# Kernel tuning notes

Hardware: AMD Instinct MI355X
Metric: run time of the kernel (lower is better)

## Reference

```python
import jax, jax.numpy as jnp
import numpy as np

NUM_K_HEADS = 16
NUM_V_HEADS = 32
DK = 128
DV = 128
KCONV = 4
EPS = 1e-6
KEY_DIM = NUM_K_HEADS * DK      # 2048
VALUE_DIM = NUM_V_HEADS * DV    # 4096
HIDDEN = 2048
T_TOKENS = 4096


def setup_inputs() -> dict:
    key = jax.random.key(0)
    ks = jax.random.split(key, 10)
    s = 0.02
    return {
        "hidden_states": jax.random.normal(ks[0], (T_TOKENS, HIDDEN), jnp.float32),
        "W_qkv": jax.random.normal(ks[1], (2 * KEY_DIM + VALUE_DIM, HIDDEN), jnp.float32) * s,
        "W_z": jax.random.normal(ks[2], (VALUE_DIM, HIDDEN), jnp.float32) * s,
        "W_b": jax.random.normal(ks[3], (NUM_V_HEADS, HIDDEN), jnp.float32) * s,
        "W_a": jax.random.normal(ks[4], (NUM_V_HEADS, HIDDEN), jnp.float32) * s,
        "conv_weight": jax.random.normal(ks[5], (2 * KEY_DIM + VALUE_DIM, KCONV), jnp.float32) * 0.2,
        "dt_bias": jnp.ones((NUM_V_HEADS,), jnp.float32),
        "A_log": jax.random.normal(ks[6], (NUM_V_HEADS,), jnp.float32) * 0.5,
        "norm_weight": jnp.ones((DV,), jnp.float32),
        "W_out": jax.random.normal(ks[7], (HIDDEN, VALUE_DIM), jnp.float32) * s,
    }


def _l2norm(x):
    return x * jax.lax.rsqrt(jnp.sum(x * x, axis=-1, keepdims=True) + 1e-6)


def _gdn_forward(hidden_states, W_qkv, W_z, W_b, W_a, conv_weight,
                 dt_bias, A_log, norm_weight, W_out):
    T = hidden_states.shape[0]
    # input projections
    mixed_qkv = hidden_states @ W_qkv.T                         # [T, 2K+V]
    z = (hidden_states @ W_z.T).reshape(T, NUM_V_HEADS, DV)     # gate
    b = hidden_states @ W_b.T                                   # [T, Hv]
    a = hidden_states @ W_a.T                                   # [T, Hv]

    # depthwise causal conv1d (kernel 4) + silu, no bias
    xp = jnp.pad(mixed_qkv, ((KCONV - 1, 0), (0, 0)))
    conv = sum(xp[i:i + T] * conv_weight[:, i] for i in range(KCONV))
    x = jax.nn.silu(conv)

    q = x[:, :KEY_DIM].reshape(T, NUM_K_HEADS, DK)
    k = x[:, KEY_DIM:2 * KEY_DIM].reshape(T, NUM_K_HEADS, DK)
    v = x[:, 2 * KEY_DIM:].reshape(T, NUM_V_HEADS, DV)

    rep = NUM_V_HEADS // NUM_K_HEADS  # grouped value attention: repeat q/k heads
    q = jnp.repeat(_l2norm(q), rep, axis=1)  # [T, Hv, DK]
    k = jnp.repeat(_l2norm(k), rep, axis=1)

    beta = jax.nn.sigmoid(b)                                   # [T, Hv]
    g = -jnp.exp(A_log) * jax.nn.softplus(a + dt_bias)         # [T, Hv] log-decay
    scale = DK ** -0.5

    def step(S, inp):
        qt, kt, vt, bt, gt = inp
        S = S * jnp.exp(gt)[:, None, None]                     # gated decay
        kv = jnp.einsum('hk,hkv->hv', kt, S)                   # memory readout
        delta = (vt - kv) * bt[:, None]                        # delta rule update
        S = S + jnp.einsum('hk,hv->hkv', kt, delta)
        ot = jnp.einsum('hk,hkv->hv', qt, S) * scale
        return S, ot

    S0 = jnp.zeros((NUM_V_HEADS, DK, DV), mixed_qkv.dtype)
    _, o = jax.lax.scan(step, S0, (q, k, v, beta, g))          # o: [T, Hv, DV]

    # gated RMSNorm (norm before gate)
    var = jnp.mean(o * o, axis=-1, keepdims=True)
    on = o * jax.lax.rsqrt(var + EPS) * norm_weight
    y = on * jax.nn.silu(z)

    return y.reshape(T, VALUE_DIM) @ W_out.T                   # [T, HIDDEN]


def reference(hidden_states, W_qkv, W_z, W_b, W_a, conv_weight,
              dt_bias, A_log, norm_weight, W_out):
    return _gdn_forward(hidden_states, W_qkv, W_z, W_b, W_a, conv_weight,
                        dt_bias, A_log, norm_weight, W_out)
```

## Files before the change

kernel.cpp:

```cpp
#include <hip/hip_runtime.h>
#include <cstdint>
#include <cstddef>

typedef __bf16 bf16_t;
typedef __bf16 bf16x8 __attribute__((ext_vector_type(8)));
typedef __bf16 bf16x4 __attribute__((ext_vector_type(4)));
typedef float floatx4 __attribute__((ext_vector_type(4)));

__device__ __forceinline__ void async16(const bf16_t* g, bf16_t* l) {
  __builtin_amdgcn_global_load_lds(
      (const __attribute__((address_space(1))) unsigned int*)g,
      (__attribute__((address_space(3))) unsigned int*)l, 16, 0, 0);
}

__device__ __forceinline__ void barrier_lds() {
  asm volatile("s_waitcnt lgkmcnt(0)\n\ts_barrier" ::: "memory");
}

__device__ __forceinline__ float siluf(float x) { return x / (1.f + __expf(-x)); }

#define MFMA16(a, b, c) __builtin_amdgcn_mfma_f32_16x16x32_bf16(a, b, c, 0, 0, 0)

__global__ __launch_bounds__(256) void k_cvt(const float* __restrict__ in,
                                             bf16_t* __restrict__ out, int n4) {
  int i = blockIdx.x * 256 + threadIdx.x;
  if (i >= n4) return;
  const float4 f = ((const float4*)in)[i];
  bf16x4 r;
  r[0] = (bf16_t)f.x; r[1] = (bf16_t)f.y; r[2] = (bf16_t)f.z; r[3] = (bf16_t)f.w;
  ((bf16x4*)out)[i] = r;
}

__global__ __launch_bounds__(256) void k_build_wba(const float* __restrict__ wb,
                                                   const float* __restrict__ wa,
                                                   bf16_t* __restrict__ out) {
  int i = blockIdx.x * 256 + threadIdx.x;
  int e = i * 4;
  int row = e >> 11;
  int col = e & 2047;
  float4 f = make_float4(0.f, 0.f, 0.f, 0.f);
  if (row < 32)      f = *(const float4*)&wb[row * 2048 + col];
  else if (row < 64) f = *(const float4*)&wa[(row - 32) * 2048 + col];
  bf16x4 r;
  r[0] = (bf16_t)f.x; r[1] = (bf16_t)f.y; r[2] = (bf16_t)f.z; r[3] = (bf16_t)f.w;
  *(bf16x4*)&out[e] = r;
}

template<bool OUT_BF16>
__global__ __launch_bounds__(256) void gemm_bt(const bf16_t* __restrict__ A,
                                               const bf16_t* __restrict__ B,
                                               void* __restrict__ Cout,
                                               int M, int N, int K) {
  __shared__ __align__(16) bf16_t As[4096];
  __shared__ __align__(16) bf16_t Bs[4096];
  const int tid  = threadIdx.x;
  const int lane = tid & 63;
  const int wave = tid >> 6;
  const int quad = lane >> 4;
  const int l16  = lane & 15;
  const int wr   = (wave >> 1) * 64;
  const int wc   = (wave & 1) * 64;
  const int m0   = blockIdx.y * 128;
  const int n0   = blockIdx.x * 128;
  const int ra   = tid >> 2;
  const int ca   = (tid & 3) * 8;

  const bf16_t* gA = A + (size_t)(m0 + ra) * K + ca;
  const bf16_t* gB = B + (size_t)(n0 + ra) * K + ca;
  bf16_t* lA = &As[tid * 8];
  bf16_t* lB = &Bs[tid * 8];

  floatx4 acc[4][4] = {};

  for (int k0 = 0; k0 < K; k0 += 32) {
    __syncthreads();
    async16(gA + k0, lA);
    async16(gA + k0 + (size_t)64 * K, lA + 2048);
    async16(gB + k0, lB);
    async16(gB + k0 + (size_t)64 * K, lB + 2048);
    __syncthreads();
    bf16x8 af[4], bfr[4];
#pragma unroll
    for (int i = 0; i < 4; ++i) {
      af[i]  = *(const bf16x8*)&As[(wr + i * 16 + l16) * 32 + quad * 8];
      bfr[i] = *(const bf16x8*)&Bs[(wc + i * 16 + l16) * 32 + quad * 8];
    }
#pragma unroll
    for (int mi = 0; mi < 4; ++mi)
#pragma unroll
      for (int ni = 0; ni < 4; ++ni)
        acc[mi][ni] = MFMA16(af[mi], bfr[ni], acc[mi][ni]);
  }

#pragma unroll
  for (int mi = 0; mi < 4; ++mi) {
#pragma unroll
    for (int ni = 0; ni < 4; ++ni) {
      const int row = m0 + wr + mi * 16 + quad * 4;
      const int col = n0 + wc + ni * 16 + l16;
#pragma unroll
      for (int r = 0; r < 4; ++r) {
        if (OUT_BF16)
          ((bf16_t*)Cout)[(size_t)(row + r) * N + col] = (bf16_t)acc[mi][ni][r];
        else
          ((float*)Cout)[(size_t)(row + r) * N + col] = acc[mi][ni][r];
      }
    }
  }
}

__global__ __launch_bounds__(256) void k_betag(const float* __restrict__ cba,
                                               const float* __restrict__ A_log,
                                               const float* __restrict__ dtb,
                                               float* __restrict__ beta_t,
                                               float* __restrict__ g_t) {
  int i = blockIdx.x * 256 + threadIdx.x;
  int t = i >> 5, h = i & 31;
  float b = cba[t * 128 + h];
  float a = cba[t * 128 + 32 + h];
  beta_t[h * 4096 + t] = 1.f / (1.f + __expf(-b));
  float x = a + dtb[h];
  float sp = (x > 20.f) ? x : log1pf(__expf(x));
  g_t[h * 4096 + t] = -__expf(A_log[h]) * sp;
}

__global__ __launch_bounds__(64) void k_conv(const bf16_t* __restrict__ mixed,
                                             const float* __restrict__ cw,
                                             bf16_t* __restrict__ qo,
                                             bf16_t* __restrict__ ko,
                                             bf16_t* __restrict__ vo) {
  const int grp = blockIdx.x;
  const int t0 = blockIdx.y * 8;
  const int l = threadIdx.x;
  const int c0 = grp * 128 + l;
  const int c1 = c0 + 64;
  const float4 w0 = *(const float4*)&cw[c0 * 4];
  const float4 w1 = *(const float4*)&cw[c1 * 4];
  float h0[3], h1[3];
#pragma unroll
  for (int j = 0; j < 3; ++j) {
    int tt = t0 - 3 + j;
    h0[j] = (tt >= 0) ? (float)mixed[(size_t)tt * 8192 + c0] : 0.f;
    h1[j] = (tt >= 0) ? (float)mixed[(size_t)tt * 8192 + c1] : 0.f;
  }
#pragma unroll
  for (int i = 0; i < 8; ++i) {
    const int t = t0 + i;
    float x0 = (float)mixed[(size_t)t * 8192 + c0];
    float x1 = (float)mixed[(size_t)t * 8192 + c1];
    float a0 = w0.x * h0[0] + w0.y * h0[1] + w0.z * h0[2] + w0.w * x0;
    float a1 = w1.x * h1[0] + w1.y * h1[1] + w1.z * h1[2] + w1.w * x1;
    h0[0] = h0[1]; h0[1] = h0[2]; h0[2] = x0;
    h1[0] = h1[1]; h1[1] = h1[2]; h1[2] = x1;
    float v0 = siluf(a0), v1 = siluf(a1);
    if (grp < 32) {
      float s = v0 * v0 + v1 * v1;
#pragma unroll
      for (int m = 1; m < 64; m <<= 1) s += __shfl_xor(s, m);
      float r = rsqrtf(s + 1e-6f);
      if (grp < 16) {
        bf16_t* q = qo + ((size_t)t * 16 + grp) * 128;
        q[l]      = (bf16_t)(v0 * r * 0.08838834764831845f);
        q[l + 64] = (bf16_t)(v1 * r * 0.08838834764831845f);
      } else {
        bf16_t* k = ko + ((size_t)t * 16 + grp - 16) * 128;
        k[l]      = (bf16_t)(v0 * r);
        k[l + 64] = (bf16_t)(v1 * r);
      }
    } else {
      bf16_t* v = vo + ((size_t)t * 32 + grp - 32) * 128;
      v[l]      = (bf16_t)v0;
      v[l + 64] = (bf16_t)v1;
    }
  }
}

__global__ __launch_bounds__(256, 2) void k_prep(
    const bf16_t* __restrict__ qg, const bf16_t* __restrict__ kg,
    const bf16_t* __restrict__ vg,
    const float* __restrict__ bb_t, const float* __restrict__ gb_t,
    bf16_t* __restrict__ Vt, bf16_t* __restrict__ Wlo, bf16_t* __restrict__ Whi,
    bf16_t* __restrict__ Mout, bf16_t* __restrict__ kt, float* __restrict__ smalls) {
  const int c = blockIdx.x >> 5;
  const int h = blockIdx.x & 31;
  const int kh = h >> 1;
  const int t0 = c * 64;
  const int tid = threadIdx.x, lane = tid & 63, wave = tid >> 6;
  const int quad = lane >> 4, l16 = lane & 15;

  __shared__ __align__(16) bf16_t lsKQ[2][64][136];
  __shared__ float lsC[64][68];
  __shared__ float lsG[64], lsA[64], lsSc[64], lsBeta[64];

  {
    const int r = tid >> 2, s0 = (tid & 3) * 32;
    const bf16_t* kr = kg + ((size_t)(t0 + r) * 16 + kh) * 128 + s0;
    const bf16_t* qr = qg + ((size_t)(t0 + r) * 16 + kh) * 128 + s0;
#pragma unroll
    for (int j = 0; j < 4; ++j) {
      *(uint4*)&lsKQ[0][r][s0 + j * 8] = *(const uint4*)&kr[j * 8];
      *(uint4*)&lsKQ[1][r][s0 + j * 8] = *(const uint4*)&qr[j * 8];
    }
  }
  if (wave == 0) {
    float gv = gb_t[(size_t)h * 4096 + t0 + lane];
#pragma unroll
    for (int off = 1; off < 64; off <<= 1) {
      float n = __shfl_up(gv, off);
      if (lane >= off) gv += n;
    }
    float GL = __shfl(gv, 63);
    lsG[lane] = gv;
    lsA[lane] = __expf(gv);
    lsSc[lane] = __expf(GL - gv);
    lsBeta[lane] = bb_t[(size_t)h * 4096 + t0 + lane];
  }
  __syncthreads();

  const int mr = (wave >> 1) * 32, nr = (wave & 1) * 32;
  floatx4 ak[2][2] = {}, aq[2][2] = {};
  if (wave != 1) {
#pragma unroll
    for (int ks = 0; ks < 4; ++ks) {
      bf16x8 yf[2], xk[2], xq[2];
#pragma unroll
      for (int i = 0; i < 2; ++i) {
        yf[i] = *(const bf16x8*)&lsKQ[0][nr + i * 16 + l16][ks * 32 + quad * 8];
        xk[i] = *(const bf16x8*)&lsKQ[0][mr + i * 16 + l16][ks * 32 + quad * 8];
        xq[i] = *(const bf16x8*)&lsKQ[1][mr + i * 16 + l16][ks * 32 + quad * 8];
      }
#pragma unroll
      for (int i = 0; i < 2; ++i)
#pragma unroll
        for (int j = 0; j < 2; ++j) {
          ak[i][j] = MFMA16(xk[i], yf[j], ak[i][j]);
          aq[i][j] = MFMA16(xq[i], yf[j], aq[i][j]);
        }
    }
  }
  bf16_t* Mb = Mout + (size_t)(h * 64 + c) * 4096;
#pragma unroll
  for (int i = 0; i < 2; ++i)
#pragma unroll
    for (int j = 0; j < 2; ++j)
#pragma unroll
      for (int r = 0; r < 4; ++r) {
        int t = mr + i * 16 + quad * 4 + r;
        int s = nr + j * 16 + l16;
        float e = __expf(lsG[t] - lsG[s]);
        float cv = (s < t) ? lsBeta[t] * e * ak[i][j][r] : 0.f;
        float mv = (s <= t) ? e * aq[i][j][r] : 0.f;
        if (wave != 1) lsC[t][s] = cv;
        Mb[t * 64 + s] = (bf16_t)mv;
      }
  __syncthreads();

  const int col = tid & 127;
  const bool isW = tid >= 128;
  float vals[64];
#pragma unroll
  for (int t = 0; t < 64; ++t) {
    float b;
    if (!isW) b = (float)vg[((size_t)(t0 + t) * 32 + h) * 128 + col];
    else      b = lsA[t] * (float)lsKQ[0][t][col];
    vals[t] = lsBeta[t] * b;
  }
#pragma unroll
  for (int t = 1; t < 64; ++t) {
    float acc = vals[t];
#pragma unroll
    for (int s4 = 0; s4 <= (t - 1) >> 2; ++s4) {
      float4 cv = *(const float4*)&lsC[t][s4 * 4];
      acc -= cv.x * vals[s4 * 4 + 0];
      acc -= cv.y * vals[s4 * 4 + 1];
      acc -= cv.z * vals[s4 * 4 + 2];
      acc -= cv.w * vals[s4 * 4 + 3];
    }
    vals[t] = acc;
  }

  if (!isW) {
    bf16_t* vd = Vt + (size_t)(h * 64 + c) * 8192 + (size_t)col * 64;
#pragma unroll
    for (int j = 0; j < 16; ++j) {
      bf16x4 p;
      p[0] = (bf16_t)vals[j * 4 + 0];
      p[1] = (bf16_t)vals[j * 4 + 1];
      p[2] = (bf16_t)vals[j * 4 + 2];
      p[3] = (bf16_t)vals[j * 4 + 3];
      *(bf16x4*)&vd[j * 4] = p;
    }
  } else {
#pragma unroll
    for (int t = 0; t < 64; ++t) vals[t] = -vals[t];
  }

  if ((h & 1) == 0) {
    const int dk = tid >> 1, sh = (tid & 1) * 32;
    bf16_t* kd = kt + (size_t)(c * 16 + kh) * 8192 + (size_t)dk * 64 + sh;
#pragma unroll
    for (int j4 = 0; j4 < 4; ++j4) {
      bf16x8 v;
#pragma unroll
      for (int e = 0; e < 8; ++e) v[e] = lsKQ[0][sh + j4 * 8 + e][dk];
      *(bf16x8*)&kd[j4 * 8] = v;
    }
  }
  if (tid < 64) {
    float* sm = smalls + (size_t)(h * 64 + c) * 128;
    sm[tid] = lsA[tid];
    sm[64 + tid] = lsSc[tid];
  }
  __syncthreads();

  bf16_t* lsT = &lsKQ[0][0][0];
  if (isW) {
#pragma unroll
    for (int t = 0; t < 64; ++t) lsT[t * 272 + tid] = (bf16_t)vals[t];
  }
  __syncthreads();

  {
    const int r = tid >> 2, part = tid & 3;
    const bf16_t* src = &lsT[r * 272 + 128 + part * 32];
    bf16_t* Wb = (h < 16 ? Wlo : Whi) + (size_t)((h & 15) * 64 + c) * 8192 + r * 128 + part * 32;
#pragma unroll
    for (int j = 0; j < 4; ++j)
      *(uint4*)&Wb[j * 8] = *(const uint4*)&src[j * 8];
  }
}

__device__ __forceinline__ void chain_prefetch(
    int c2, int wave, int l16, int quad, int trow, int dv0, int kh,
    const bf16_t* __restrict__ Wbase, const bf16_t* __restrict__ Vbase,
    const bf16_t* __restrict__ Mbase, const bf16_t* __restrict__ qg,
    const bf16_t* __restrict__ ktg, const float* __restrict__ Sbase,
    bf16x8 nW[4], bf16x8 nQ[4], bf16x8 nK[4], bf16x8 nM[2],
    bf16x4 nV[4], float4& nA, float4& nSc, float& nAL) {
  const bf16_t* Wn = Wbase + (size_t)c2 * 8192;
  const bf16_t* Vn = Vbase + (size_t)c2 * 8192;
  const bf16_t* Qn = qg + ((size_t)(c2 * 64 + wave * 16 + l16) * 16 + kh) * 128;
  const bf16_t* Kn = ktg + (size_t)(c2 * 16 + kh) * 8192;
  const bf16_t* Mn = Mbase + (size_t)c2 * 4096 + (wave * 16 + l16) * 64;
  const float* sm = Sbase + (size_t)c2 * 128;
#pragma unroll
  for (int ks = 0; ks < 4; ++ks) {
    nW[ks] = *(const bf16x8*)&Wn[(size_t)(wave * 16 + l16) * 128 + ks * 32 + quad * 8];
    nQ[ks] = *(const bf16x8*)&Qn[ks * 32 + quad * 8];
    nK[ks] = *(const bf16x8*)&Kn[(size_t)((wave + 4 * (ks >> 1)) * 16 + l16) * 64 + (ks & 1) * 32 + quad * 8];
  }
#pragma unroll
  for (int ks = 0; ks < 2; ++ks) nM[ks] = *(const bf16x8*)&Mn[ks * 32 + quad * 8];
#pragma unroll
  for (int tn = 0; tn < 4; ++tn)
    nV[tn] = *(const bf16x4*)&Vn[(size_t)(dv0 + tn * 16 + l16) * 64 + trow];
  nA = *(const float4*)&sm[trow];
  nSc = *(const float4*)&sm[64 + trow];
  nAL = sm[63];
}

__global__ __launch_bounds__(256, 1) void k_chain(
    const bf16_t* __restrict__ qg, const bf16_t* __restrict__ VtT,
    const bf16_t* __restrict__ Wlo, const bf16_t* __restrict__ Whi,
    const bf16_t* __restrict__ Mg, const bf16_t* __restrict__ ktg,
    const float* __restrict__ smalls, bf16_t* __restrict__ o) {
  const int h = blockIdx.x & 31;
  const int dv0 = (blockIdx.x >> 5) * 64;
  const int kh = h >> 1;
  const int tid = threadIdx.x, lane = tid & 63, wave = tid >> 6;
  const int quad = lane >> 4, l16 = lane & 15;
  const int trow = wave * 16 + quad * 4;

  __shared__ __align__(16) bf16_t lsXT[64][72];
  __shared__ __align__(16) bf16_t lsXbT[64][72];
  __shared__ __align__(16) bf16_t lsS[64][136];

  const bf16_t* Wbase = (h < 16 ? Wlo : Whi) + (size_t)(h & 15) * 64 * 8192;
  const bf16_t* Vbase = VtT + (size_t)h * 64 * 8192;
  const bf16_t* Mbase = Mg + (size_t)h * 64 * 4096;
  const float*  Sbase = smalls + (size_t)h * 64 * 128;

  floatx4 sacc[2][4] = {};
  for (int i = tid; i < 64 * 136; i += 256) (&lsS[0][0])[i] = (bf16_t)0.f;

  bf16x8 nW[4], nQ[4], nK[4], nM[2];
  bf16x4 nV[4];
  float4 nA, nSc;
  float nAL;
  chain_prefetch(0, wave, l16, quad, trow, dv0, kh, Wbase, Vbase, Mbase, qg, ktg,
                 Sbase, nW, nQ, nK, nM, nV, nA, nSc, nAL);
  __syncthreads();

  for (int cc = 0; cc < 64; ++cc) {
    const int t0 = cc * 64;
    bf16x8 cW[4], cQ[4], cK[4], cM[2];
    float cV[16];
    float4 cA = nA, cSc = nSc;
    float cAL = nAL;
#pragma unroll
    for (int ks = 0; ks < 4; ++ks) { cW[ks] = nW[ks]; cQ[ks] = nQ[ks]; cK[ks] = nK[ks]; }
    cM[0] = nM[0]; cM[1] = nM[1];
#pragma unroll
    for (int tn = 0; tn < 4; ++tn)
#pragma unroll
      for (int r = 0; r < 4; ++r) cV[tn * 4 + r] = (float)nV[tn][r];

    if (cc + 1 < 64)
      chain_prefetch(cc + 1, wave, l16, quad, trow, dv0, kh, Wbase, Vbase, Mbase,
                     qg, ktg, Sbase, nW, nQ, nK, nM, nV, nA, nSc, nAL);

    bf16x8 bS[4][4];
#pragma unroll
    for (int ks = 0; ks < 4; ++ks)
#pragma unroll
      for (int tn = 0; tn < 4; ++tn)
        bS[ks][tn] = *(const bf16x8*)&lsS[tn * 16 + l16][ks * 32 + quad * 8];
    floatx4 xacc[4];
#pragma unroll
    for (int tn = 0; tn < 4; ++tn)
#pragma unroll
      for (int r = 0; r < 4; ++r) xacc[tn][r] = cV[tn * 4 + r];
#pragma unroll
    for (int ks = 0; ks < 4; ++ks)
#pragma unroll
      for (int tn = 0; tn < 4; ++tn)
        xacc[tn] = MFMA16(cW[ks], bS[ks][tn], xacc[tn]);
#pragma unroll
    for (int tn = 0; tn < 4; ++tn) {
      bf16x4 px, pb;
#pragma unroll
      for (int r = 0; r < 4; ++r) {
        px[r] = (bf16_t)xacc[tn][r];
        pb[r] = (bf16_t)(xacc[tn][r] * ((const float*)&cSc)[r]);
      }
      *(bf16x4*)&lsXT[tn * 16 + l16][trow] = px;
      *(bf16x4*)&lsXbT[tn * 16 + l16][trow] = pb;
    }
    barrier_lds();

    floatx4 qacc[4] = {};
#pragma unroll
    for (int ks = 0; ks < 4; ++ks)
#pragma unroll
      for (int tn = 0; tn < 4; ++tn)
        qacc[tn] = MFMA16(cQ[ks], bS[ks][tn], qacc[tn]);
#pragma unroll
    for (int tn = 0; tn < 4; ++tn)
#pragma unroll
      for (int r = 0; r < 4; ++r) qacc[tn][r] *= ((const float*)&cA)[r];
#pragma unroll
    for (int ks = 0; ks < 2; ++ks)
#pragma unroll
      for (int tn = 0; tn < 4; ++tn) {
        bf16x8 bX = *(const bf16x8*)&lsXT[tn * 16 + l16][ks * 32 + quad * 8];
        qacc[tn] = MFMA16(cM[ks], bX, qacc[tn]);
      }
#pragma unroll
    for (int tn = 0; tn < 4; ++tn)
#pragma unroll
      for (int r = 0; r < 4; ++r)
        o[((size_t)(t0 + trow + r) * 32 + h) * 128 + dv0 + tn * 16 + l16] =
            (bf16_t)qacc[tn][r];
#pragma unroll
    for (int mh = 0; mh < 2; ++mh)
#pragma unroll
      for (int tn = 0; tn < 4; ++tn)
#pragma unroll
        for (int r = 0; r < 4; ++r) sacc[mh][tn][r] *= cAL;
#pragma unroll
    for (int ks = 0; ks < 2; ++ks) {
      bf16x8 bXb[4];
#pragma unroll
      for (int tn = 0; tn < 4; ++tn)
        bXb[tn] = *(const bf16x8*)&lsXbT[tn * 16 + l16][ks * 32 + quad * 8];
#pragma unroll
      for (int mh = 0; mh < 2; ++mh)
#pragma unroll
        for (int tn = 0; tn < 4; ++tn)
          sacc[mh][tn] = MFMA16(cK[mh * 2 + ks], bXb[tn], sacc[mh][tn]);
    }
#pragma unroll
    for (int mh = 0; mh < 2; ++mh)
#pragma unroll
      for (int tn = 0; tn < 4; ++tn) {
        bf16x4 ps;
#pragma unroll
        for (int r = 0; r < 4; ++r) ps[r] = (bf16_t)sacc[mh][tn][r];
        *(bf16x4*)&lsS[tn * 16 + l16][(wave + 4 * mh) * 16 + quad * 4] = ps;
      }
    barrier_lds();
  }
}

__global__ __launch_bounds__(256) void k_gate(const bf16_t* __restrict__ o,
                                              const bf16_t* __restrict__ z,
                                              const float* __restrict__ nw,
                                              bf16_t* __restrict__ y) {
  const int row = blockIdx.x * 4 + (threadIdx.x >> 6);
  const int l = threadIdx.x & 63;
  const bf16_t* orow = o + (size_t)row * 128;
  float o0 = (float)orow[l], o1 = (float)orow[l + 64];
  float s = o0 * o0 + o1 * o1;
#pragma unroll
  for (int m = 1; m < 64; m <<= 1) s += __shfl_xor(s, m);
  float r = rsqrtf(s * (1.f / 128.f) + 1e-6f);
  const bf16_t* zrow = z + (size_t)row * 128;
  float z0 = (float)zrow[l], z1 = (float)zrow[l + 64];
  bf16_t* yrow = y + (size_t)row * 128;
  yrow[l]      = (bf16_t)(o0 * r * nw[l] * siluf(z0));
  yrow[l + 64] = (bf16_t)(o1 * r * nw[l + 64] * siluf(z1));
}

extern "C" void kernel_launch(void* const* d_in, const int* in_sizes, int n_in,
                              void* d_out, int out_size, void* d_ws, size_t ws_size,
                              hipStream_t stream) {
  const float* hidden = (const float*)d_in[0];
  const float* W_qkv  = (const float*)d_in[1];
  const float* W_z    = (const float*)d_in[2];
  const float* W_b    = (const float*)d_in[3];
  const float* W_a    = (const float*)d_in[4];
  const float* conv_w = (const float*)d_in[5];
  const float* dt_b   = (const float*)d_in[6];
  const float* A_log  = (const float*)d_in[7];
  const float* norm_w = (const float*)d_in[8];
  const float* W_out  = (const float*)d_in[9];
  float* out = (float*)d_out;

  char* w = (char*)d_ws;
  const size_t MB = 1024 * 1024;
  bf16_t* hs    = (bf16_t*)(w + 0 * MB);
  bf16_t* Wlo   = hs;
  bf16_t* wqkv  = (bf16_t*)(w + 16 * MB);
  bf16_t* Vtb   = wqkv;
  bf16_t* ybuf  = wqkv;
  bf16_t* wz    = (bf16_t*)(w + 48 * MB);
  bf16_t* Whi   = wz;
  bf16_t* wout  = (bf16_t*)(w + 64 * MB);
  bf16_t* wba   = (bf16_t*)(w + 80 * MB);
  bf16_t* mixed = (bf16_t*)(w + 81 * MB);
  bf16_t* obuf  = mixed;
  bf16_t* Mbuf  = (bf16_t*)(w + 113 * MB);
  bf16_t* ktb   = (bf16_t*)(w + 129 * MB);
  bf16_t* zbuf  = (bf16_t*)(w + 145 * MB);
  float*  cba   = (float*)(w + 177 * MB);
  float*  smalls= cba;
  bf16_t* qb    = (bf16_t*)(w + 179 * MB);
  bf16_t* kb    = (bf16_t*)(w + 195 * MB);
  bf16_t* vb    = (bf16_t*)(w + 211 * MB);
  float*  betab = (float*)(w + 243 * MB);
  float*  gbuf  = (float*)(w + 243 * MB + 512 * 1024);

  k_cvt<<<8192, 256, 0, stream>>>(hidden, hs, 2097152);
  k_cvt<<<16384, 256, 0, stream>>>(W_qkv, wqkv, 4194304);
  k_cvt<<<8192, 256, 0, stream>>>(W_z, wz, 2097152);
  k_cvt<<<8192, 256, 0, stream>>>(W_out, wout, 2097152);
  k_build_wba<<<256, 256, 0, stream>>>(W_b, W_a, wba);

  gemm_bt<true><<<dim3(64, 32), 256, 0, stream>>>(hs, wqkv, mixed, 4096, 8192, 2048);
  gemm_bt<true><<<dim3(32, 32), 256, 0, stream>>>(hs, wz, zbuf, 4096, 4096, 2048);
  gemm_bt<false><<<dim3(1, 32), 256, 0, stream>>>(hs, wba, cba, 4096, 128, 2048);
  k_betag<<<512, 256, 0, stream>>>(cba, A_log, dt_b, betab, gbuf);

  k_conv<<<dim3(64, 512), 64, 0, stream>>>(mixed, conv_w, qb, kb, vb);

  k_prep<<<2048, 256, 0, stream>>>(qb, kb, vb, betab, gbuf,
                                   Vtb, Wlo, Whi, Mbuf, ktb, smalls);
  k_chain<<<64, 256, 0, stream>>>(qb, Vtb, Wlo, Whi, Mbuf, ktb, smalls, obuf);

  k_gate<<<32768, 256, 0, stream>>>(obuf, zbuf, norm_w, ybuf);
  gemm_bt<false><<<dim3(16, 32), 256, 0, stream>>>(ybuf, wout, out, 4096, 2048, 4096);
}
```

Measured before the change: 977.4 us.

## Add 256x256-tile 8-wave GEMM with 4-stage async LDS pipeline for input projections

Adds a new bf16 GEMM kernel that uses 256x256 output tiles, 512 threads and 128KB of dynamic LDS with a 4-deep async global-to-LDS ring. It also uses swizzled LDS layouts, XCD-aware block remapping and s_setprio around the MFMA bursts. The kernel is used for the QKV and Z projections to raise operand reuse and overlap loads with compute relative to the older 128-tile GEMM. The trade is high register and LDS use, which allows only one block per CU, and fewer workgroups: 512 and 256, against 256 CUs.

```diff
diff --git a/kernel.cpp b/kernel.cpp
--- a/kernel.cpp
+++ b/kernel.cpp
@@ -109,6 +109,126 @@
   }
 }
 
+template<bool OUT_BF16>
+__global__ __launch_bounds__(512, 1) void gemm256(const bf16_t* __restrict__ A,
+                                                  const bf16_t* __restrict__ B,
+                                                  void* __restrict__ Cout,
+                                                  int M, int N, int K) {
+  extern __shared__ __align__(16) bf16_t sm[];
+  const int tid  = threadIdx.x;
+  const int lane = tid & 63;
+  const int wave = tid >> 6;
+  const int quad = lane >> 4;
+  const int l16  = lane & 15;
+  const int wm   = wave >> 2;
+  const int wn   = wave & 3;
+
+  const int gx  = (int)gridDim.x;
+  const int nwg = gx * (int)gridDim.y;
+  const int id  = (int)blockIdx.y * gx + (int)blockIdx.x;
+  const int cpx = nwg >> 3;
+  const int sw  = (id & 7) * cpx + (id >> 3);
+  const int m0  = (sw / gx) * 256;
+  const int n0  = (sw % gx) * 256;
+
+  const int lr    = lane >> 2;
+  const int lslot = (lane & 3) ^ ((lane >> 3) & 3);
+  const bf16_t* gA = A + (size_t)(m0 + wave * 32 + lr) * K + lslot * 8;
+  const bf16_t* gB = B + (size_t)(n0 + wave * 32 + lr) * K + lslot * 8;
+  const int ldsA0 = wave * 1024 + lane * 8;
+  const int ldsB0 = 8192 + wave * 1024 + lane * 8;
+
+#define STG_A(u, kt) {                                          \
+    bf16_t* la = sm + (u) * 16384 + ldsA0;                      \
+    const bf16_t* ga = gA + (size_t)(kt) * 32;                  \
+    async16(ga, la);                                            \
+    async16(ga + (size_t)16 * K, la + 512); }
+#define STG_B(u, kt) {                                          \
+    bf16_t* lb = sm + (u) * 16384 + ldsB0;                      \
+    const bf16_t* gb = gB + (size_t)(kt) * 32;                  \
+    async16(gb, lb);                                            \
+    async16(gb + (size_t)16 * K, lb + 512); }
+
+  int offA[8], offB[4];
+#pragma unroll
+  for (int i = 0; i < 8; ++i) {
+    int ra = wm * 128 + i * 16 + l16;
+    offA[i] = (ra * 32 + quad * 8) ^ (((ra >> 1) & 3) << 3);
+  }
+#pragma unroll
+  for (int i = 0; i < 4; ++i) {
+    int rb = wn * 64 + i * 16 + l16;
+    offB[i] = 8192 + ((rb * 32 + quad * 8) ^ (((rb >> 1) & 3) << 3));
+  }
+
+  floatx4 acc[8][4] = {};
+  const int KT = K >> 5;
+
+  STG_A(0, 0); STG_B(0, 0);
+  STG_A(1, 1); STG_B(1, 1);
+  STG_A(2, 2); STG_B(2, 2);
+  asm volatile("s_waitcnt vmcnt(8)" ::: "memory");
+  asm volatile("s_barrier" ::: "memory");
+
+  for (int U = 0; U < KT; ++U) {
+    const int bu = U & 3;
+    const bf16_t* sb = sm + bu * 16384;
+    const int un = U + 3;
+    const int tu = un & 3;
+    bf16x8 af[4], bfr[4];
+
+#pragma unroll
+    for (int i = 0; i < 4; ++i) {
+      af[i]  = *(const bf16x8*)&sb[offA[i]];
+      bfr[i] = *(const bf16x8*)&sb[offB[i]];
+    }
+    if (un < KT) STG_A(tu, un);
+    asm volatile("s_barrier" ::: "memory");
+    __builtin_amdgcn_s_setprio(1);
+#pragma unroll
+    for (int mi = 0; mi < 4; ++mi)
+#pragma unroll
+      for (int ni = 0; ni < 4; ++ni)
+        acc[mi][ni] = MFMA16(af[mi], bfr[ni], acc[mi][ni]);
+    __builtin_amdgcn_s_setprio(0);
+    asm volatile("s_barrier" ::: "memory");
+
+#pragma unroll
+    for (int i = 0; i < 4; ++i) af[i] = *(const bf16x8*)&sb[offA[4 + i]];
+    if (un < KT) STG_B(tu, un);
+    if (un < KT)         asm volatile("s_waitcnt vmcnt(8)" ::: "memory");
+    else if (U + 2 < KT) asm volatile("s_waitcnt vmcnt(4)" ::: "memory");
+    else                 asm volatile("s_waitcnt vmcnt(0)" ::: "memory");
+    asm volatile("s_barrier" ::: "memory");
+    __builtin_amdgcn_s_setprio(1);
+#pragma unroll
+    for (int mi = 0; mi < 4; ++mi)
+#pragma unroll
+      for (int ni = 0; ni < 4; ++ni)
+        acc[4 + mi][ni] = MFMA16(af[mi], bfr[ni], acc[4 + mi][ni]);
+    __builtin_amdgcn_s_setprio(0);
+    asm volatile("s_barrier" ::: "memory");
+  }
+#undef STG_A
+#undef STG_B
+
+#pragma unroll
+  for (int mi = 0; mi < 8; ++mi) {
+#pragma unroll
+    for (int ni = 0; ni < 4; ++ni) {
+      const int row = m0 + wm * 128 + mi * 16 + quad * 4;
+      const int col = n0 + wn * 64 + ni * 16 + l16;
+#pragma unroll
+      for (int r = 0; r < 4; ++r) {
+        if (OUT_BF16)
+          ((bf16_t*)Cout)[(size_t)(row + r) * N + col] = (bf16_t)acc[mi][ni][r];
+        else
+          ((float*)Cout)[(size_t)(row + r) * N + col] = acc[mi][ni][r];
+      }
+    }
+  }
+}
+
 __global__ __launch_bounds__(256) void k_betag(const float* __restrict__ cba,
                                                const float* __restrict__ A_log,
                                                const float* __restrict__ dtb,
@@ -525,6 +645,15 @@
   const float* norm_w = (const float*)d_in[8];
   const float* W_out  = (const float*)d_in[9];
   float* out = (float*)d_out;
+
+  static int gemm_attr_done = 0;
+  if (!gemm_attr_done) {
+    hipFuncSetAttribute(reinterpret_cast<const void*>(&gemm256<true>),
+                        hipFuncAttributeMaxDynamicSharedMemorySize, 131072);
+    hipFuncSetAttribute(reinterpret_cast<const void*>(&gemm256<false>),
+                        hipFuncAttributeMaxDynamicSharedMemorySize, 131072);
+    gemm_attr_done = 1;
+  }
 
   char* w = (char*)d_ws;
   const size_t MB = 1024 * 1024;
@@ -556,8 +685,8 @@
   k_cvt<<<8192, 256, 0, stream>>>(W_out, wout, 2097152);
   k_build_wba<<<256, 256, 0, stream>>>(W_b, W_a, wba);
 
-  gemm_bt<true><<<dim3(64, 32), 256, 0, stream>>>(hs, wqkv, mixed, 4096, 8192, 2048);
-  gemm_bt<true><<<dim3(32, 32), 256, 0, stream>>>(hs, wz, zbuf, 4096, 4096, 2048);
+  gemm256<true><<<dim3(32, 16), 512, 131072, stream>>>(hs, wqkv, mixed, 4096, 8192, 2048);
+  gemm256<true><<<dim3(16, 16), 512, 131072, stream>>>(hs, wz, zbuf, 4096, 4096, 2048);
   gemm_bt<false><<<dim3(1, 32), 256, 0, stream>>>(hs, wba, cba, 4096, 128, 2048);
   k_betag<<<512, 256, 0, stream>>>(cba, A_log, dt_b, betab, gbuf);
 
```

After: 904.3 us. 1.08x faster.
